# Kernel tuning notes

Measured on AMD Instinct MI355X. Metric: run time of the kernel, lower is better.

## Reference

```python
import jax, jax.numpy as jnp
import numpy as np

D_MODEL = 1024
N_HEADS = 16
HEAD_DIM = D_MODEL // N_HEADS
EPS = 1e-6


def setup_inputs() -> dict:
    key = jax.random.key(0)
    k1, k2, k3 = jax.random.split(key, 3)
    b, l, d = 2, 2048, D_MODEL
    x = jax.random.normal(k1, (b, l, d), dtype=jnp.float32)
    # Linear weights stored so that y = x @ W (no bias), matching torch math
    w_qkv = jax.random.normal(k2, (d, 3 * d), dtype=jnp.float32) * (1.0 / np.sqrt(d))
    w_proj = jax.random.normal(k3, (d, d), dtype=jnp.float32) * (1.0 / np.sqrt(d))
    norm_w = jnp.ones((d,), dtype=jnp.float32)
    return {"x": x, "norm_w": norm_w, "w_qkv": w_qkv, "w_proj": w_proj}


def rms_norm(x, w, eps=EPS):
    x32 = x.astype(jnp.float32)
    inv_rms = jax.lax.rsqrt(jnp.mean(x32 * x32, axis=-1, keepdims=True) + eps)
    return (x32 * inv_rms).astype(x.dtype) * w.astype(x.dtype)


def reference(x, norm_w, w_qkv, w_proj):
    b, l, d = x.shape
    h = rms_norm(x, norm_w)
    qkv = h @ w_qkv                       # [b, l, 3d]
    q, k, v = jnp.split(qkv, 3, axis=-1)

    def heads(t):
        return t.reshape(b, l, N_HEADS, HEAD_DIM).transpose(0, 2, 1, 3)  # [b,h,l,hd]

    q, k, v = heads(q), heads(k), heads(v)
    scale = 1.0 / np.sqrt(HEAD_DIM)
    scores = jnp.einsum('bhqd,bhkd->bhqk', q, k) * scale  # full LxL scores
    attn = jax.nn.softmax(scores, axis=-1)
    ctx = jnp.einsum('bhqk,bhkd->bhqd', attn, v)
    ctx = ctx.transpose(0, 2, 1, 3).reshape(b, l, d)
    out = ctx @ w_proj
    return x + out
```

## Files before the change

### kernel.cpp

```cpp
#include <hip/hip_runtime.h>
#include <hip/hip_bf16.h>
#include <cstdint>
#include <cstddef>

typedef __attribute__((ext_vector_type(8))) short bf16x8;
typedef __attribute__((ext_vector_type(4))) float f32x4;
typedef __attribute__((ext_vector_type(16))) float f32x16;

#define GLD_LDS16(gptr, lptr)                                                  \
  __builtin_amdgcn_global_load_lds(                                            \
      (const __attribute__((address_space(1))) void*)(gptr),                   \
      (__attribute__((address_space(3))) void*)(lptr), 16, 0, 0)

__device__ __forceinline__ uint32_t cvtpk(float a, float b) {
  uint32_t d;
  asm("v_cvt_pk_bf16_f32 %0, %1, %2" : "=v"(d) : "v"(a), "v"(b));
  return d;
}

__device__ __forceinline__ float xhalf_sum(float x) {
  auto r = __builtin_amdgcn_permlane32_swap(__float_as_uint(x),
                                            __float_as_uint(x), false, false);
  return __uint_as_float(r[0]) + __uint_as_float(r[1]);
}

__global__ __launch_bounds__(256) void rmsnorm_kernel(
    const float* __restrict__ x, const float* __restrict__ w,
    __hip_bfloat16* __restrict__ h) {
  const int row = blockIdx.x;
  const int tid = threadIdx.x;
  const float4 v = reinterpret_cast<const float4*>(x + (size_t)row * 1024)[tid];
  float ss = v.x * v.x + v.y * v.y + v.z * v.z + v.w * v.w;
#pragma unroll
  for (int off = 32; off >= 1; off >>= 1) ss += __shfl_down(ss, off);
  __shared__ float red[4];
  if ((tid & 63) == 0) red[tid >> 6] = ss;
  __syncthreads();
  const float inv =
      rsqrtf((red[0] + red[1] + red[2] + red[3]) * (1.0f / 1024.0f) + 1e-6f);
  const float4 wv = reinterpret_cast<const float4*>(w)[tid];
  __hip_bfloat16* hp = h + (size_t)row * 1024 + tid * 4;
  hp[0] = __float2bfloat16(v.x * inv * wv.x);
  hp[1] = __float2bfloat16(v.y * inv * wv.y);
  hp[2] = __float2bfloat16(v.z * inv * wv.z);
  hp[3] = __float2bfloat16(v.w * inv * wv.w);
}

__global__ __launch_bounds__(256) void transpose_cast2_kernel(
    const float* __restrict__ w_qkv, const float* __restrict__ w_proj,
    __hip_bfloat16* __restrict__ wqkvT, __hip_bfloat16* __restrict__ wprojT) {
  __shared__ float tile[32][33];
  const float* src;
  __hip_bfloat16* dst;
  int C, bx;
  if (blockIdx.x < 96) {
    src = w_qkv; dst = wqkvT; C = 3072; bx = blockIdx.x * 32;
  } else {
    src = w_proj; dst = wprojT; C = 1024; bx = (blockIdx.x - 96) * 32;
  }
  const int R = 1024;
  const int by = blockIdx.y * 32;
  const int tx = threadIdx.x;
  const int ty = threadIdx.y;
#pragma unroll
  for (int j = 0; j < 32; j += 8)
    tile[ty + j][tx] = src[(size_t)(by + ty + j) * C + bx + tx];
  __syncthreads();
#pragma unroll
  for (int j = 0; j < 32; j += 8)
    dst[(size_t)(bx + ty + j) * R + by + tx] = __float2bfloat16(tile[tx][ty + j]);
}

template <int BM, int BN, int RESID>
__device__ __forceinline__ void gemm_tile(
    const __hip_bfloat16* __restrict__ A, const __hip_bfloat16* __restrict__ BT,
    void* __restrict__ Cout, const float* __restrict__ resid, int M, int N,
    int K, int bx, int by, __hip_bfloat16* As, __hip_bfloat16* Bs) {
  const int tid = threadIdx.x;
  const int lane = tid & 63;
  const int wid = tid >> 6;
  const int m0 = by * BM;
  const int n0 = bx * BN;
  const int wr = wid >> 1, wc = wid & 1;
  constexpr int MI = BM / 32, NJ = BN / 32;
  f32x4 acc[MI][NJ] = {};
  const int nk = K >> 6;
  const int lr = lane & 15, lk = lane >> 4;
  const int srow = lane >> 2;
  const int scol = (lane & 3) * 8;
  for (int kt = 0; kt < nk; ++kt) {
#pragma unroll
    for (int it = 0; it < BM / 32; ++it) {
      const int c = wid + it * 4;
      const int sub = c / (BM / 16), cc = c % (BM / 16);
      GLD_LDS16(A + (size_t)(m0 + cc * 16 + srow) * K + kt * 64 + sub * 32 + scol,
                As + c * 512);
    }
#pragma unroll
    for (int it = 0; it < BN / 32; ++it) {
      const int c = wid + it * 4;
      const int sub = c / (BN / 16), cc = c % (BN / 16);
      GLD_LDS16(BT + (size_t)(n0 + cc * 16 + srow) * K + kt * 64 + sub * 32 + scol,
                Bs + c * 512);
    }
    __syncthreads();
    bf16x8 af[MI][2], bfr[NJ][2];
#pragma unroll
    for (int i = 0; i < MI; ++i)
#pragma unroll
      for (int s = 0; s < 2; ++s)
        af[i][s] = *(const bf16x8*)(As + s * (BM * 32) +
                                    (wr * (BM / 2) + i * 16 + lr) * 32 + lk * 8);
#pragma unroll
    for (int j = 0; j < NJ; ++j)
#pragma unroll
      for (int s = 0; s < 2; ++s)
        bfr[j][s] = *(const bf16x8*)(Bs + s * (BN * 32) +
                                     (wc * (BN / 2) + j * 16 + lr) * 32 + lk * 8);
#pragma unroll
    for (int s = 0; s < 2; ++s)
#pragma unroll
      for (int i = 0; i < MI; ++i)
#pragma unroll
        for (int j = 0; j < NJ; ++j)
          acc[i][j] = __builtin_amdgcn_mfma_f32_16x16x32_bf16(
              af[i][s], bfr[j][s], acc[i][j], 0, 0, 0);
    __syncthreads();
  }
#pragma unroll
  for (int i = 0; i < MI; ++i)
#pragma unroll
    for (int j = 0; j < NJ; ++j)
#pragma unroll
      for (int r = 0; r < 4; ++r) {
        const int row = m0 + wr * (BM / 2) + i * 16 + lk * 4 + r;
        const int col = n0 + wc * (BN / 2) + j * 16 + lr;
        const float v = acc[i][j][r];
        if (RESID) {
          ((float*)Cout)[(size_t)row * N + col] =
              resid[(size_t)row * N + col] + v;
        } else {
          ((__hip_bfloat16*)Cout)[(size_t)row * N + col] = __float2bfloat16(v);
        }
      }
}

__global__ __launch_bounds__(256) void qkv_gemm_kernel(
    const __hip_bfloat16* __restrict__ h, const __hip_bfloat16* __restrict__ wqkT,
    const __hip_bfloat16* __restrict__ wvT, __hip_bfloat16* __restrict__ qkbuf,
    __hip_bfloat16* __restrict__ vTbuf) {
  __shared__ __align__(16) __hip_bfloat16 As[128 * 64];
  __shared__ __align__(16) __hip_bfloat16 Bs[128 * 64];
  const int bid = blockIdx.x;
  if (bid < 512) {
    const int xcd = bid & 7, seq = bid >> 3;
    const int by = (xcd >> 1) * 8 + (seq >> 3);
    const int bx = (xcd & 1) * 8 + (seq & 7);
    gemm_tile<128, 128, 0>(h, wqkT, (void*)qkbuf, nullptr, 4096, 2048, 1024,
                           bx, by, As, Bs);
  } else {
    const int t = bid - 512;
    const int xcd = t & 7, seq = t >> 3;
    const int by = seq >> 2;
    const int bx = xcd * 4 + (seq & 3);
    gemm_tile<128, 128, 0>(wvT, h, (void*)vTbuf, nullptr, 1024, 4096, 1024, bx,
                           by, As, Bs);
  }
}

__global__ __launch_bounds__(256) void proj_gemm_kernel(
    const __hip_bfloat16* __restrict__ ctx, const __hip_bfloat16* __restrict__ wpT,
    float* __restrict__ out, const float* __restrict__ x) {
  __shared__ __align__(16) __hip_bfloat16 As[128 * 64];
  __shared__ __align__(16) __hip_bfloat16 Bs[64 * 64];
  const int bid = blockIdx.x;
  const int xcd = bid & 7, seq = bid >> 3;
  const int by = xcd * 4 + (seq >> 4);
  const int bx = seq & 15;
  gemm_tile<128, 64, 1>(ctx, wpT, (void*)out, x, 4096, 1024, 1024, bx, by, As,
                        Bs);
}

__global__ __launch_bounds__(128) void attn_kernel(
    const __hip_bfloat16* __restrict__ qk, const __hip_bfloat16* __restrict__ vT,
    __hip_bfloat16* __restrict__ ctx) {
  const int flat = blockIdx.x;
  const int xcd = flat & 7, seq = flat >> 3;
  const int bh = xcd * 4 + (seq >> 4);
  const int qt = seq & 15;
  const int b = bh >> 4, h = bh & 15;
  const int tid = threadIdx.x, lane = tid & 63, wid = tid >> 6;
  const size_t tok0 = (size_t)b * 2048;
  const int q0 = qt * 128 + wid * 64;
  const int l31 = lane & 31;
  const int hi = lane >> 5;

  __shared__ __align__(16) char Kl[2][64 * 128];
  __shared__ __align__(16) char Vl[2][64 * 128];

  const int sr = tid >> 1;
  const int scE = (tid & 1) * 32;
  const int scB = (tid & 1) * 64;
  const int swW = (sr & 7) << 4;

  const __hip_bfloat16* kbase = qk + tok0 * 2048 + 1024 + (size_t)h * 64;
  const __hip_bfloat16* vbase = vT + ((size_t)(h * 64 + sr)) * 4096 + tok0;

  bf16x8 qfA[4], qfB[4];
  {
    const float c = 0.125f * 1.44269504f;
    const __hip_bfloat16* qA = qk + (tok0 + q0 + l31) * 2048 + h * 64 + hi * 8;
    const __hip_bfloat16* qB =
        qk + (tok0 + q0 + 32 + l31) * 2048 + h * 64 + hi * 8;
#pragma unroll
    for (int ks = 0; ks < 4; ++ks) {
      bf16x8 va = *(const bf16x8*)(qA + ks * 16);
      bf16x8 vb = *(const bf16x8*)(qB + ks * 16);
      const __hip_bfloat16* ia = (const __hip_bfloat16*)&va;
      const __hip_bfloat16* ib = (const __hip_bfloat16*)&vb;
      __hip_bfloat16* oa = (__hip_bfloat16*)&qfA[ks];
      __hip_bfloat16* ob = (__hip_bfloat16*)&qfB[ks];
#pragma unroll
      for (int i = 0; i < 8; ++i) {
        oa[i] = __float2bfloat16(__bfloat162float(ia[i]) * c);
        ob[i] = __float2bfloat16(__bfloat162float(ib[i]) * c);
      }
    }
  }

  const int swR = (l31 & 7) << 4;
  const int rb0 = l31 * 128;
  const int rb1 = (32 + l31) * 128;

  bf16x8 kr[4], vr[4];
  auto load_tile = [&](int t) {
    const __hip_bfloat16* kp = kbase + (size_t)(t * 64 + sr) * 2048 + scE;
    const __hip_bfloat16* vp = vbase + t * 64 + scE;
#pragma unroll
    for (int k = 0; k < 4; ++k) kr[k] = *(const bf16x8*)(kp + 8 * k);
#pragma unroll
    for (int k = 0; k < 4; ++k) vr[k] = *(const bf16x8*)(vp + 8 * k);
  };
  auto write_tile = [&](int bf) {
#pragma unroll
    for (int k = 0; k < 4; ++k) {
      const int off = sr * 128 + ((scB + 16 * k) ^ swW);
      *(bf16x8*)(Kl[bf] + off) = kr[k];
      *(bf16x8*)(Vl[bf] + off) = vr[k];
    }
  };

  f32x16 oA0 = {}, oA1 = {}, oB0 = {}, oB1 = {};
  float lA = 0.f, lB = 0.f;

  load_tile(0);
  write_tile(0);
  __syncthreads();

  for (int kvt = 0; kvt < 32; ++kvt) {
    const int cur = kvt & 1;
    if (kvt + 1 < 32) load_tile(kvt + 1);

    f32x16 sA0 = {}, sA1 = {}, sB0 = {}, sB1 = {};
#pragma unroll
    for (int ks = 0; ks < 4; ++ks) {
      const int cOff = (ks * 32 + hi * 16) ^ swR;
      const bf16x8 kf0 = *(const bf16x8*)(Kl[cur] + rb0 + cOff);
      const bf16x8 kf1 = *(const bf16x8*)(Kl[cur] + rb1 + cOff);
      sA0 = __builtin_amdgcn_mfma_f32_32x32x16_bf16(kf0, qfA[ks], sA0, 0, 0, 0);
      sA1 = __builtin_amdgcn_mfma_f32_32x32x16_bf16(kf1, qfA[ks], sA1, 0, 0, 0);
      sB0 = __builtin_amdgcn_mfma_f32_32x32x16_bf16(kf0, qfB[ks], sB0, 0, 0, 0);
      sB1 = __builtin_amdgcn_mfma_f32_32x32x16_bf16(kf1, qfB[ks], sB1, 0, 0, 0);
    }

    float psA = 0.f, psB = 0.f;
    uint32_t pA0[8], pA1[8], pB0[8], pB1[8];
#pragma unroll
    for (int i = 0; i < 8; ++i) {
      const float a0 = __builtin_amdgcn_exp2f(sA0[2 * i]);
      const float a1 = __builtin_amdgcn_exp2f(sA0[2 * i + 1]);
      const float a2 = __builtin_amdgcn_exp2f(sA1[2 * i]);
      const float a3 = __builtin_amdgcn_exp2f(sA1[2 * i + 1]);
      psA += (a0 + a1) + (a2 + a3);
      pA0[i] = cvtpk(a0, a1);
      pA1[i] = cvtpk(a2, a3);
      const float b0 = __builtin_amdgcn_exp2f(sB0[2 * i]);
      const float b1 = __builtin_amdgcn_exp2f(sB0[2 * i + 1]);
      const float b2 = __builtin_amdgcn_exp2f(sB1[2 * i]);
      const float b3 = __builtin_amdgcn_exp2f(sB1[2 * i + 1]);
      psB += (b0 + b1) + (b2 + b3);
      pB0[i] = cvtpk(b0, b1);
      pB1[i] = cvtpk(b2, b3);
    }
    lA += psA;
    lB += psB;

#pragma unroll
    for (int ts = 0; ts < 4; ++ts) {
      const int cOff = (ts * 32 + hi * 16) ^ swR;
      const bf16x8 vf0 = *(const bf16x8*)(Vl[cur] + rb0 + cOff);
      const bf16x8 vf1 = *(const bf16x8*)(Vl[cur] + rb1 + cOff);
      const int o = (ts & 1) * 4;
      {
        const uint32_t* pk = (ts < 2) ? pA0 : pA1;
        auto w02 =
            __builtin_amdgcn_permlane32_swap(pk[o], pk[o + 2], false, false);
        auto w13 =
            __builtin_amdgcn_permlane32_swap(pk[o + 1], pk[o + 3], false, false);
        uint32_t fr[4] = {w02[0], w13[0], w02[1], w13[1]};
        const bf16x8 pf = *(const bf16x8*)fr;
        oA0 = __builtin_amdgcn_mfma_f32_32x32x16_bf16(vf0, pf, oA0, 0, 0, 0);
        oA1 = __builtin_amdgcn_mfma_f32_32x32x16_bf16(vf1, pf, oA1, 0, 0, 0);
      }
      {
        const uint32_t* pk = (ts < 2) ? pB0 : pB1;
        auto w02 =
            __builtin_amdgcn_permlane32_swap(pk[o], pk[o + 2], false, false);
        auto w13 =
            __builtin_amdgcn_permlane32_swap(pk[o + 1], pk[o + 3], false, false);
        uint32_t fr[4] = {w02[0], w13[0], w02[1], w13[1]};
        const bf16x8 pf = *(const bf16x8*)fr;
        oB0 = __builtin_amdgcn_mfma_f32_32x32x16_bf16(vf0, pf, oB0, 0, 0, 0);
        oB1 = __builtin_amdgcn_mfma_f32_32x32x16_bf16(vf1, pf, oB1, 0, 0, 0);
      }
    }

    if (kvt + 1 < 32) write_tile(cur ^ 1);
    __syncthreads();
  }

#pragma unroll
  for (int qb = 0; qb < 2; ++qb) {
    const float lrow = xhalf_sum(qb ? lB : lA);
    const float linv = 1.0f / lrow;
    __hip_bfloat16* cb =
        ctx + (tok0 + q0 + qb * 32 + l31) * 1024 + h * 64;
    const f32x16& o0 = qb ? oB0 : oA0;
    const f32x16& o1 = qb ? oB1 : oA1;
#pragma unroll
    for (int dh = 0; dh < 2; ++dh) {
#pragma unroll
      for (int rq = 0; rq < 4; ++rq) {
        const int d0 = 8 * rq + 4 * hi + 32 * dh;
        float v0, v1, v2, v3;
        if (dh) {
          v0 = o1[4 * rq];
          v1 = o1[4 * rq + 1];
          v2 = o1[4 * rq + 2];
          v3 = o1[4 * rq + 3];
        } else {
          v0 = o0[4 * rq];
          v1 = o0[4 * rq + 1];
          v2 = o0[4 * rq + 2];
          v3 = o0[4 * rq + 3];
        }
        *(uint32_t*)(cb + d0) = cvtpk(v0 * linv, v1 * linv);
        *(uint32_t*)(cb + d0 + 2) = cvtpk(v2 * linv, v3 * linv);
      }
    }
  }
}

extern "C" void kernel_launch(void* const* d_in, const int* in_sizes, int n_in,
                              void* d_out, int out_size, void* d_ws,
                              size_t ws_size, hipStream_t stream) {
  const float* x = (const float*)d_in[0];
  const float* norm_w = (const float*)d_in[1];
  const float* w_qkv = (const float*)d_in[2];
  const float* w_proj = (const float*)d_in[3];
  float* out = (float*)d_out;

  char* ws = (char*)d_ws;
  __hip_bfloat16* hbuf = (__hip_bfloat16*)(ws);
  __hip_bfloat16* wqkvT = (__hip_bfloat16*)(ws + (size_t)8 * 1024 * 1024);
  __hip_bfloat16* wprojT = (__hip_bfloat16*)(ws + (size_t)14 * 1024 * 1024);
  __hip_bfloat16* qkbuf = (__hip_bfloat16*)(ws + (size_t)16 * 1024 * 1024);
  __hip_bfloat16* vTbuf = (__hip_bfloat16*)(ws + (size_t)32 * 1024 * 1024);
  __hip_bfloat16* ctx = (__hip_bfloat16*)(ws + (size_t)40 * 1024 * 1024);

  rmsnorm_kernel<<<dim3(4096), dim3(256), 0, stream>>>(x, norm_w, hbuf);
  transpose_cast2_kernel<<<dim3(128, 32), dim3(32, 8), 0, stream>>>(
      w_qkv, w_proj, wqkvT, wprojT);
  qkv_gemm_kernel<<<dim3(768), dim3(256), 0, stream>>>(
      hbuf, wqkvT, wqkvT + (size_t)2048 * 1024, qkbuf, vTbuf);
  attn_kernel<<<dim3(512), dim3(128), 0, stream>>>(qkbuf, vTbuf, ctx);
  proj_gemm_kernel<<<dim3(512), dim3(256), 0, stream>>>(ctx, wprojT, out, x);
}
```

Before: 126.8 us.

## Split attention KV range across wave pairs and stage tiles with direct-to-LDS loads

The attention kernel now runs 256 threads per block. Two wave pairs each process half of the key/value sequence, staging K and V tiles into swizzled LDS with asynchronous global_load_lds instead of register round-trips. The partial outputs and row sums are then combined through LDS before normalization. The GEMM tiles also drop from a K-step of 64 to 32 with a simpler contiguous staging layout, which halves their LDS footprint but doubles the number of barriers per tile. The split-KV merge adds the two halves' outputs and sums directly, so it is only correct if both halves use a common softmax reference (no per-half running max), and it adds an extra LDS reduction and sync.

```diff
diff --git a/kernel.cpp b/kernel.cpp
--- a/kernel.cpp
+++ b/kernel.cpp
@@ -83,48 +83,39 @@
   const int n0 = bx * BN;
   const int wr = wid >> 1, wc = wid & 1;
   constexpr int MI = BM / 32, NJ = BN / 32;
+  constexpr int NCHA = BM / 16, NCHB = BN / 16;
   f32x4 acc[MI][NJ] = {};
-  const int nk = K >> 6;
+  const int nk = K >> 5;
   const int lr = lane & 15, lk = lane >> 4;
-  const int srow = lane >> 2;
-  const int scol = (lane & 3) * 8;
   for (int kt = 0; kt < nk; ++kt) {
 #pragma unroll
-    for (int it = 0; it < BM / 32; ++it) {
+    for (int it = 0; it < NCHA / 4; ++it) {
       const int c = wid + it * 4;
-      const int sub = c / (BM / 16), cc = c % (BM / 16);
-      GLD_LDS16(A + (size_t)(m0 + cc * 16 + srow) * K + kt * 64 + sub * 32 + scol,
+      const int e = c * 512 + lane * 8;
+      GLD_LDS16(A + (size_t)(m0 + (e >> 5)) * K + kt * 32 + (e & 31),
                 As + c * 512);
     }
 #pragma unroll
-    for (int it = 0; it < BN / 32; ++it) {
+    for (int it = 0; it < NCHB / 4; ++it) {
       const int c = wid + it * 4;
-      const int sub = c / (BN / 16), cc = c % (BN / 16);
-      GLD_LDS16(BT + (size_t)(n0 + cc * 16 + srow) * K + kt * 64 + sub * 32 + scol,
+      const int e = c * 512 + lane * 8;
+      GLD_LDS16(BT + (size_t)(n0 + (e >> 5)) * K + kt * 32 + (e & 31),
                 Bs + c * 512);
     }
     __syncthreads();
-    bf16x8 af[MI][2], bfr[NJ][2];
+    bf16x8 af[MI], bfr[NJ];
 #pragma unroll
     for (int i = 0; i < MI; ++i)
-#pragma unroll
-      for (int s = 0; s < 2; ++s)
-        af[i][s] = *(const bf16x8*)(As + s * (BM * 32) +
-                                    (wr * (BM / 2) + i * 16 + lr) * 32 + lk * 8);
+      af[i] = *(const bf16x8*)(As + (wr * (BM / 2) + i * 16 + lr) * 32 + lk * 8);
 #pragma unroll
     for (int j = 0; j < NJ; ++j)
-#pragma unroll
-      for (int s = 0; s < 2; ++s)
-        bfr[j][s] = *(const bf16x8*)(Bs + s * (BN * 32) +
-                                     (wc * (BN / 2) + j * 16 + lr) * 32 + lk * 8);
-#pragma unroll
-    for (int s = 0; s < 2; ++s)
-#pragma unroll
-      for (int i = 0; i < MI; ++i)
-#pragma unroll
-        for (int j = 0; j < NJ; ++j)
-          acc[i][j] = __builtin_amdgcn_mfma_f32_16x16x32_bf16(
-              af[i][s], bfr[j][s], acc[i][j], 0, 0, 0);
+      bfr[j] = *(const bf16x8*)(Bs + (wc * (BN / 2) + j * 16 + lr) * 32 + lk * 8);
+#pragma unroll
+    for (int i = 0; i < MI; ++i)
+#pragma unroll
+      for (int j = 0; j < NJ; ++j)
+        acc[i][j] = __builtin_amdgcn_mfma_f32_16x16x32_bf16(af[i], bfr[j],
+                                                            acc[i][j], 0, 0, 0);
     __syncthreads();
   }
 #pragma unroll
@@ -149,8 +140,8 @@
     const __hip_bfloat16* __restrict__ h, const __hip_bfloat16* __restrict__ wqkT,
     const __hip_bfloat16* __restrict__ wvT, __hip_bfloat16* __restrict__ qkbuf,
     __hip_bfloat16* __restrict__ vTbuf) {
-  __shared__ __align__(16) __hip_bfloat16 As[128 * 64];
-  __shared__ __align__(16) __hip_bfloat16 Bs[128 * 64];
+  __shared__ __align__(16) __hip_bfloat16 As[128 * 32];
+  __shared__ __align__(16) __hip_bfloat16 Bs[128 * 32];
   const int bid = blockIdx.x;
   if (bid < 512) {
     const int xcd = bid & 7, seq = bid >> 3;
@@ -171,8 +162,8 @@
 __global__ __launch_bounds__(256) void proj_gemm_kernel(
     const __hip_bfloat16* __restrict__ ctx, const __hip_bfloat16* __restrict__ wpT,
     float* __restrict__ out, const float* __restrict__ x) {
-  __shared__ __align__(16) __hip_bfloat16 As[128 * 64];
-  __shared__ __align__(16) __hip_bfloat16 Bs[64 * 64];
+  __shared__ __align__(16) __hip_bfloat16 As[128 * 32];
+  __shared__ __align__(16) __hip_bfloat16 Bs[64 * 32];
   const int bid = blockIdx.x;
   const int xcd = bid & 7, seq = bid >> 3;
   const int by = xcd * 4 + (seq >> 4);
@@ -181,7 +172,7 @@
                         Bs);
 }
 
-__global__ __launch_bounds__(128) void attn_kernel(
+__global__ __launch_bounds__(256) void attn_kernel(
     const __hip_bfloat16* __restrict__ qk, const __hip_bfloat16* __restrict__ vT,
     __hip_bfloat16* __restrict__ ctx) {
   const int flat = blockIdx.x;
@@ -190,21 +181,21 @@
   const int qt = seq & 15;
   const int b = bh >> 4, h = bh & 15;
   const int tid = threadIdx.x, lane = tid & 63, wid = tid >> 6;
+  const int half = wid >> 1, qsub = wid & 1;
   const size_t tok0 = (size_t)b * 2048;
-  const int q0 = qt * 128 + wid * 64;
+  const size_t tokH = tok0 + half * 1024;
+  const int q0 = qt * 128 + qsub * 64;
   const int l31 = lane & 31;
   const int hi = lane >> 5;
 
-  __shared__ __align__(16) char Kl[2][64 * 128];
-  __shared__ __align__(16) char Vl[2][64 * 128];
-
-  const int sr = tid >> 1;
-  const int scE = (tid & 1) * 32;
-  const int scB = (tid & 1) * 64;
-  const int swW = (sr & 7) << 4;
-
-  const __hip_bfloat16* kbase = qk + tok0 * 2048 + 1024 + (size_t)h * 64;
-  const __hip_bfloat16* vbase = vT + ((size_t)(h * 64 + sr)) * 4096 + tok0;
+  __shared__ __align__(16) char smem[65536];
+  char* Kbuf = smem + half * 32768;
+  char* Vbuf = smem + half * 32768 + 16384;
+
+  const int srowL = lane >> 3;
+  const int colE = ((lane & 7) ^ srowL) << 3;
+  const __hip_bfloat16* kbaseH = qk + tokH * 2048 + 1024 + (size_t)h * 64;
+  const __hip_bfloat16* vbaseH = vT + (size_t)h * 64 * 4096 + tokH;
 
   bf16x8 qfA[4], qfB[4];
   {
@@ -232,41 +223,33 @@
   const int rb0 = l31 * 128;
   const int rb1 = (32 + l31) * 128;
 
-  bf16x8 kr[4], vr[4];
-  auto load_tile = [&](int t) {
-    const __hip_bfloat16* kp = kbase + (size_t)(t * 64 + sr) * 2048 + scE;
-    const __hip_bfloat16* vp = vbase + t * 64 + scE;
-#pragma unroll
-    for (int k = 0; k < 4; ++k) kr[k] = *(const bf16x8*)(kp + 8 * k);
-#pragma unroll
-    for (int k = 0; k < 4; ++k) vr[k] = *(const bf16x8*)(vp + 8 * k);
-  };
-  auto write_tile = [&](int bf) {
-#pragma unroll
-    for (int k = 0; k < 4; ++k) {
-      const int off = sr * 128 + ((scB + 16 * k) ^ swW);
-      *(bf16x8*)(Kl[bf] + off) = kr[k];
-      *(bf16x8*)(Vl[bf] + off) = vr[k];
+  auto stage_tile = [&](int bf, int t) {
+#pragma unroll
+    for (int i = 0; i < 4; ++i) {
+      const int c = qsub * 4 + i;
+      GLD_LDS16(kbaseH + (size_t)(t * 64 + c * 8 + srowL) * 2048 + colE,
+                Kbuf + bf * 8192 + c * 1024);
+      GLD_LDS16(vbaseH + (size_t)(c * 8 + srowL) * 4096 + t * 64 + colE,
+                Vbuf + bf * 8192 + c * 1024);
     }
   };
 
   f32x16 oA0 = {}, oA1 = {}, oB0 = {}, oB1 = {};
   float lA = 0.f, lB = 0.f;
 
-  load_tile(0);
-  write_tile(0);
+  stage_tile(0, 0);
   __syncthreads();
 
-  for (int kvt = 0; kvt < 32; ++kvt) {
-    const int cur = kvt & 1;
-    if (kvt + 1 < 32) load_tile(kvt + 1);
+  for (int t = 0; t < 16; ++t) {
+    const int cur = t & 1;
+    if (t + 1 < 16) stage_tile(cur ^ 1, t + 1);
 
     f32x16 sA0 = {}, sA1 = {}, sB0 = {}, sB1 = {};
 #pragma unroll
     for (int ks = 0; ks < 4; ++ks) {
       const int cOff = (ks * 32 + hi * 16) ^ swR;
-      const bf16x8 kf0 = *(const bf16x8*)(Kl[cur] + rb0 + cOff);
-      const bf16x8 kf1 = *(const bf16x8*)(Kl[cur] + rb1 + cOff);
+      const bf16x8 kf0 = *(const bf16x8*)(Kbuf + cur * 8192 + rb0 + cOff);
+      const bf16x8 kf1 = *(const bf16x8*)(Kbuf + cur * 8192 + rb1 + cOff);
       sA0 = __builtin_amdgcn_mfma_f32_32x32x16_bf16(kf0, qfA[ks], sA0, 0, 0, 0);
       sA1 = __builtin_amdgcn_mfma_f32_32x32x16_bf16(kf1, qfA[ks], sA1, 0, 0, 0);
       sB0 = __builtin_amdgcn_mfma_f32_32x32x16_bf16(kf0, qfB[ks], sB0, 0, 0, 0);
@@ -298,8 +281,8 @@
 #pragma unroll
     for (int ts = 0; ts < 4; ++ts) {
       const int cOff = (ts * 32 + hi * 16) ^ swR;
-      const bf16x8 vf0 = *(const bf16x8*)(Vl[cur] + rb0 + cOff);
-      const bf16x8 vf1 = *(const bf16x8*)(Vl[cur] + rb1 + cOff);
+      const bf16x8 vf0 = *(const bf16x8*)(Vbuf + cur * 8192 + rb0 + cOff);
+      const bf16x8 vf1 = *(const bf16x8*)(Vbuf + cur * 8192 + rb1 + cOff);
       const int o = (ts & 1) * 4;
       {
         const uint32_t* pk = (ts < 2) ? pA0 : pA1;
@@ -325,37 +308,73 @@
       }
     }
 
-    if (kvt + 1 < 32) write_tile(cur ^ 1);
     __syncthreads();
   }
 
-#pragma unroll
-  for (int qb = 0; qb < 2; ++qb) {
-    const float lrow = xhalf_sum(qb ? lB : lA);
-    const float linv = 1.0f / lrow;
-    __hip_bfloat16* cb =
-        ctx + (tok0 + q0 + qb * 32 + l31) * 1024 + h * 64;
-    const f32x16& o0 = qb ? oB0 : oA0;
-    const f32x16& o1 = qb ? oB1 : oA1;
-#pragma unroll
-    for (int dh = 0; dh < 2; ++dh) {
-#pragma unroll
-      for (int rq = 0; rq < 4; ++rq) {
-        const int d0 = 8 * rq + 4 * hi + 32 * dh;
-        float v0, v1, v2, v3;
-        if (dh) {
-          v0 = o1[4 * rq];
-          v1 = o1[4 * rq + 1];
-          v2 = o1[4 * rq + 2];
-          v3 = o1[4 * rq + 3];
-        } else {
-          v0 = o0[4 * rq];
-          v1 = o0[4 * rq + 1];
-          v2 = o0[4 * rq + 2];
-          v3 = o0[4 * rq + 3];
+  float* osh = (float*)smem;
+  float* lsh = (float*)(smem + 48 * 1024);
+  if (half == 1) {
+    float* dst = osh + (qsub * 64 + lane) * 68;
+    f32x4* d4 = (f32x4*)dst;
+    const f32x4* pa0 = (const f32x4*)&oA0;
+    const f32x4* pa1 = (const f32x4*)&oA1;
+    const f32x4* pb0 = (const f32x4*)&oB0;
+    const f32x4* pb1 = (const f32x4*)&oB1;
+#pragma unroll
+    for (int k = 0; k < 4; ++k) {
+      d4[k] = pa0[k];
+      d4[4 + k] = pa1[k];
+      d4[8 + k] = pb0[k];
+      d4[12 + k] = pb1[k];
+    }
+    lsh[(qsub * 64 + lane) * 2] = lA;
+    lsh[(qsub * 64 + lane) * 2 + 1] = lB;
+  }
+  __syncthreads();
+  if (half == 0) {
+    const float* src = osh + (qsub * 64 + lane) * 68;
+    const f32x4* s4 = (const f32x4*)src;
+    f32x4* pa0 = (f32x4*)&oA0;
+    f32x4* pa1 = (f32x4*)&oA1;
+    f32x4* pb0 = (f32x4*)&oB0;
+    f32x4* pb1 = (f32x4*)&oB1;
+#pragma unroll
+    for (int k = 0; k < 4; ++k) {
+      pa0[k] += s4[k];
+      pa1[k] += s4[4 + k];
+      pb0[k] += s4[8 + k];
+      pb1[k] += s4[12 + k];
+    }
+    lA += lsh[(qsub * 64 + lane) * 2];
+    lB += lsh[(qsub * 64 + lane) * 2 + 1];
+
+#pragma unroll
+    for (int qb = 0; qb < 2; ++qb) {
+      const float lrow = xhalf_sum(qb ? lB : lA);
+      const float linv = 1.0f / lrow;
+      __hip_bfloat16* cb = ctx + (tok0 + q0 + qb * 32 + l31) * 1024 + h * 64;
+      const f32x16& o0 = qb ? oB0 : oA0;
+      const f32x16& o1 = qb ? oB1 : oA1;
+#pragma unroll
+      for (int dh = 0; dh < 2; ++dh) {
+#pragma unroll
+        for (int rq = 0; rq < 4; ++rq) {
+          const int d0 = 8 * rq + 4 * hi + 32 * dh;
+          float v0, v1, v2, v3;
+          if (dh) {
+            v0 = o1[4 * rq];
+            v1 = o1[4 * rq + 1];
+            v2 = o1[4 * rq + 2];
+            v3 = o1[4 * rq + 3];
+          } else {
+            v0 = o0[4 * rq];
+            v1 = o0[4 * rq + 1];
+            v2 = o0[4 * rq + 2];
+            v3 = o0[4 * rq + 3];
+          }
+          *(uint32_t*)(cb + d0) = cvtpk(v0 * linv, v1 * linv);
+          *(uint32_t*)(cb + d0 + 2) = cvtpk(v2 * linv, v3 * linv);
         }
-        *(uint32_t*)(cb + d0) = cvtpk(v0 * linv, v1 * linv);
-        *(uint32_t*)(cb + d0 + 2) = cvtpk(v2 * linv, v3 * linv);
       }
     }
   }
@@ -383,6 +402,6 @@
       w_qkv, w_proj, wqkvT, wprojT);
   qkv_gemm_kernel<<<dim3(768), dim3(256), 0, stream>>>(
       hbuf, wqkvT, wqkvT + (size_t)2048 * 1024, qkbuf, vTbuf);
-  attn_kernel<<<dim3(512), dim3(128), 0, stream>>>(qkbuf, vTbuf, ctx);
+  attn_kernel<<<dim3(512), dim3(256), 0, stream>>>(qkbuf, vTbuf, ctx);
   proj_gemm_kernel<<<dim3(512), dim3(256), 0, stream>>>(ctx, wprojT, out, x);
 }
```

Measured after the change: 114.2 us. 10.0% less time.
